# Kernel tuning notes

Hardware: AMD Instinct MI355X
Metric: run time of the kernel (lower is better)

The kernel has to match this reference:

```python
import jax, jax.numpy as jnp
import numpy as np

OUTPUT_SIZE = 65
THRESHOLD = 0.2
EPS = 1e-6


def setup_inputs() -> dict:
    key = jax.random.key(0)
    x = jax.random.normal(key, (64, 4, 512), dtype=jnp.float32)
    return {"x": x}


def _valid_mask(x):
    # True from first nonzero to last nonzero along L, per (n, c); all False if row is all-zero.
    N, C, L = x.shape
    nz = x != 0
    any_nz = nz.any(axis=2, keepdims=True)            # [N, C, 1]
    first = jnp.argmax(nz, axis=2)                    # [N, C]
    last = (L - 1) - jnp.argmax(nz[:, :, ::-1], axis=2)
    idx = jnp.arange(L)
    mask = (idx[None, None, :] >= first[:, :, None]) & (idx[None, None, :] <= last[:, :, None])
    return mask & any_nz                              # [N, C, L] bool


def reference(x):
    N, C, L = x.shape
    mask = _valid_mask(x)
    mf = mask.astype(x.dtype)
    cnt = jnp.clip(mf.sum(axis=2), 1, None)           # [N, C]
    mean = (x * mf).sum(axis=2) / cnt                 # [N, C]
    var = (((x * mf - mean[..., None]) ** 2) * mf).sum(axis=2) / cnt
    std = jnp.sqrt(var)                               # [N, C]
    x_norm = (x - mean[..., None]) / jnp.clip(std, EPS, None)[..., None]
    x_norm = jnp.where(mask, x_norm, jnp.zeros((), x.dtype))  # [N, C, L]
    # Recurrence plot: cdist on 1-d points == |x_i - x_j|, thresholded.
    dist = jnp.abs(x_norm[..., :, None] - x_norm[..., None, :])  # [N, C, L, L]
    rp = (dist < THRESHOLD).astype(x.dtype)
    size = min(L, OUTPUT_SIZE)
    out = jnp.zeros((N, C, OUTPUT_SIZE, OUTPUT_SIZE), dtype=x.dtype)
    out = out.at[:, :, :size, :size].set(rp[:, :, :size, :size])
    return out
```

## Files before the change

### kernel.cpp

```cpp
#include <hip/hip_runtime.h>
#include <climits>

#define LROW 512
#define OUT_S 65
#define NOUT (OUT_S * OUT_S)
#define THRESH 0.2f
#define EPS_F 1e-6f

__global__ __launch_bounds__(256) void rp_kernel(const float* __restrict__ x,
                                                 float* __restrict__ out) {
    const int row = blockIdx.x;
    const int tid = threadIdx.x;
    const float* xr = x + (size_t)row * LROW;

    const float v0 = xr[tid];
    const float v1 = xr[tid + 256];

    int lo = INT_MAX, hi = -1;
    if (v0 != 0.0f) { lo = tid; hi = tid; }
    if (v1 != 0.0f) { lo = min(lo, tid + 256); hi = max(hi, tid + 256); }
    double s1 = (double)v0 + (double)v1;
    double s2 = (double)v0 * (double)v0 + (double)v1 * (double)v1;

    #pragma unroll
    for (int off = 32; off > 0; off >>= 1) {
        lo = min(lo, __shfl_xor(lo, off, 64));
        hi = max(hi, __shfl_xor(hi, off, 64));
        s1 += __shfl_xor(s1, off, 64);
        s2 += __shfl_xor(s2, off, 64);
    }

    __shared__ int    w_lo[4], w_hi[4];
    __shared__ double w_s1[4], w_s2[4];
    __shared__ float  xn[OUT_S];

    const int wid = tid >> 6;
    if ((tid & 63) == 0) {
        w_lo[wid] = lo; w_hi[wid] = hi; w_s1[wid] = s1; w_s2[wid] = s2;
    }
    __syncthreads();

    const int first = min(min(w_lo[0], w_lo[1]), min(w_lo[2], w_lo[3]));
    const int last  = max(max(w_hi[0], w_hi[1]), max(w_hi[2], w_hi[3]));
    const double S1 = (w_s1[0] + w_s1[1]) + (w_s1[2] + w_s1[3]);
    const double S2 = (w_s2[0] + w_s2[1]) + (w_s2[2] + w_s2[3]);

    const bool   anyNZ = (last >= 0);
    const double cnt   = anyNZ ? (double)(last - first + 1) : 1.0;
    const float  mean  = (float)(S1 / cnt);
    const double dm    = (double)mean;
    double var = (S2 - 2.0 * dm * S1 + cnt * dm * dm) / cnt;
    var = var > 0.0 ? var : 0.0;
    const float stdc = fmaxf(sqrtf((float)var), EPS_F);

    if (tid < OUT_S) {
        const bool m = anyNZ && (tid >= first) && (tid <= last);
        xn[tid] = m ? (v0 - mean) / stdc : 0.0f;
    }
    __syncthreads();

    float* orow = out + (size_t)row * NOUT;
    int k = tid;
    #pragma unroll
    for (int it = 0; it < 17; ++it) {
        if (k < NOUT) {
            const int ii = k / OUT_S;
            const int jj = k - ii * OUT_S;
            orow[k] = (fabsf(xn[ii] - xn[jj]) < THRESH) ? 1.0f : 0.0f;
        }
        k += 256;
    }
}

extern "C" void kernel_launch(void* const* d_in, const int* in_sizes, int n_in,
                              void* d_out, int out_size, void* d_ws, size_t ws_size,
                              hipStream_t stream) {
    const float* x  = (const float*)d_in[0];
    float*      out = (float*)d_out;
    const int rows  = in_sizes[0] / LROW;
    rp_kernel<<<rows, 256, 0, stream>>>(x, out);
}
```

Measured before the change: 10.59 us.

## Vectorize loads and stores, compute stats per-wave without block barriers

Each wave now loads the whole 512-element row with float4 loads and reduces the bounds and moments redundantly inside the wave, which removes the cross-wave shared-memory reduction and both __syncthreads. Each wave writes its own copy of the normalized prefix into LDS and waits on lgkmcnt instead of a barrier. Output rows are written as aligned float4 stores, with scalar head and tail elements handling the row offset that is not a multiple of 4. The cost is four times the redundant load and reduction work, plus a reliance on wave-local LDS visibility.

```diff
diff --git a/kernel.cpp b/kernel.cpp
--- a/kernel.cpp
+++ b/kernel.cpp
@@ -7,20 +7,33 @@
 #define THRESH 0.2f
 #define EPS_F 1e-6f
 
+typedef float f4 __attribute__((ext_vector_type(4)));
+
 __global__ __launch_bounds__(256) void rp_kernel(const float* __restrict__ x,
                                                  float* __restrict__ out) {
-    const int row = blockIdx.x;
-    const int tid = threadIdx.x;
+    const int row  = blockIdx.x;
+    const int tid  = threadIdx.x;
+    const int lane = tid & 63;
+    const int wid  = tid >> 6;
     const float* xr = x + (size_t)row * LROW;
+    const f4* xr4   = reinterpret_cast<const f4*>(xr);
 
-    const float v0 = xr[tid];
-    const float v1 = xr[tid + 256];
+    const f4 a = xr4[lane];
+    const f4 b = xr4[lane + 64];
 
     int lo = INT_MAX, hi = -1;
-    if (v0 != 0.0f) { lo = tid; hi = tid; }
-    if (v1 != 0.0f) { lo = min(lo, tid + 256); hi = max(hi, tid + 256); }
-    double s1 = (double)v0 + (double)v1;
-    double s2 = (double)v0 * (double)v0 + (double)v1 * (double)v1;
+    double s1 = 0.0, s2 = 0.0;
+    #pragma unroll
+    for (int e = 0; e < 4; ++e) {
+        const int   k0 = 4 * lane + e;
+        const float va = a[e];
+        if (va != 0.0f) { lo = min(lo, k0); hi = max(hi, k0); }
+        s1 += (double)va; s2 += (double)va * (double)va;
+        const int   k1 = k0 + 256;
+        const float vb = b[e];
+        if (vb != 0.0f) { lo = min(lo, k1); hi = max(hi, k1); }
+        s1 += (double)vb; s2 += (double)vb * (double)vb;
+    }
 
     #pragma unroll
     for (int off = 32; off > 0; off >>= 1) {
@@ -30,45 +43,58 @@
         s2 += __shfl_xor(s2, off, 64);
     }
 
-    __shared__ int    w_lo[4], w_hi[4];
-    __shared__ double w_s1[4], w_s2[4];
-    __shared__ float  xn[OUT_S];
-
-    const int wid = tid >> 6;
-    if ((tid & 63) == 0) {
-        w_lo[wid] = lo; w_hi[wid] = hi; w_s1[wid] = s1; w_s2[wid] = s2;
-    }
-    __syncthreads();
-
-    const int first = min(min(w_lo[0], w_lo[1]), min(w_lo[2], w_lo[3]));
-    const int last  = max(max(w_hi[0], w_hi[1]), max(w_hi[2], w_hi[3]));
-    const double S1 = (w_s1[0] + w_s1[1]) + (w_s1[2] + w_s1[3]);
-    const double S2 = (w_s2[0] + w_s2[1]) + (w_s2[2] + w_s2[3]);
-
-    const bool   anyNZ = (last >= 0);
-    const double cnt   = anyNZ ? (double)(last - first + 1) : 1.0;
-    const float  mean  = (float)(S1 / cnt);
+    const bool   anyNZ = (hi >= 0);
+    const double cnt   = anyNZ ? (double)(hi - lo + 1) : 1.0;
+    const float  mean  = (float)(s1 / cnt);
     const double dm    = (double)mean;
-    double var = (S2 - 2.0 * dm * S1 + cnt * dm * dm) / cnt;
+    double var = (s2 - 2.0 * dm * s1 + cnt * dm * dm) / cnt;
     var = var > 0.0 ? var : 0.0;
     const float stdc = fmaxf(sqrtf((float)var), EPS_F);
 
-    if (tid < OUT_S) {
-        const bool m = anyNZ && (tid >= first) && (tid <= last);
-        xn[tid] = m ? (v0 - mean) / stdc : 0.0f;
+    __shared__ float xnw[4][68];
+    if (lane < 17) {
+        f4 w;
+        #pragma unroll
+        for (int e = 0; e < 4; ++e) {
+            const int  k = 4 * lane + e;
+            const bool m = anyNZ && (k >= lo) && (k <= hi);
+            w[e] = m ? (a[e] - mean) / stdc : 0.0f;
+        }
+        *reinterpret_cast<f4*>(&xnw[wid][4 * lane]) = w;
     }
-    __syncthreads();
+    asm volatile("s_waitcnt lgkmcnt(0)" ::: "memory");
 
+    const float* xn = xnw[wid];
     float* orow = out + (size_t)row * NOUT;
-    int k = tid;
-    #pragma unroll
-    for (int it = 0; it < 17; ++it) {
-        if (k < NOUT) {
-            const int ii = k / OUT_S;
-            const int jj = k - ii * OUT_S;
-            orow[k] = (fabsf(xn[ii] - xn[jj]) < THRESH) ? 1.0f : 0.0f;
+
+    const int h      = (4 - (row & 3)) & 3;
+    const int nbody  = (NOUT - h) >> 2;
+    const int t0     = h + (nbody << 2);
+    const int ntail  = NOUT - t0;
+
+    if (tid < h) {
+        orow[tid] = (fabsf(xn[0] - xn[tid]) < THRESH) ? 1.0f : 0.0f;
+    }
+    if (tid >= 4 && tid - 4 < ntail) {
+        const int k = t0 + (tid - 4);
+        const int i = k / OUT_S;
+        const int j = k - i * OUT_S;
+        orow[k] = (fabsf(xn[i] - xn[j]) < THRESH) ? 1.0f : 0.0f;
+    }
+
+    for (int g = tid; g < nbody; g += 256) {
+        const int e0 = h + 4 * g;
+        const int i  = e0 / OUT_S;
+        int   jj  = e0 - i * OUT_S;
+        float xii = xn[i];
+        f4 r;
+        #pragma unroll
+        for (int e = 0; e < 4; ++e) {
+            if (jj == OUT_S) { jj = 0; xii = xn[i + 1]; }
+            r[e] = (fabsf(xii - xn[jj]) < THRESH) ? 1.0f : 0.0f;
+            ++jj;
         }
-        k += 256;
+        *reinterpret_cast<f4*>(orow + e0) = r;
     }
 }
 
```

Result: slower. 10.99 us, median of 2 (+3.8%).
